# Kernel optimization log

Measured on AMD Instinct MI355X. Metric: run time of the kernel, lower is better.

Reference implementation:

```python
import jax, jax.numpy as jnp
import numpy as np

N_NODES = 100000
N_EDGES = 3200000
IN_CH = 128
HID = 128
ACT_DIM = 1


def _gcn_layer(x, W, b, src, dst, ew, n):
    # GCNConv with edge weights and self-loops already included in (src, dst, ew).
    # Symmetric normalization: norm_e = d^{-1/2}[src] * w_e * d^{-1/2}[dst]
    h = x @ W                                            # [N, F_out] dense transform first (cheap)
    deg = jax.ops.segment_sum(ew, dst, num_segments=n)   # weighted in-degree
    dinv = jnp.where(deg > 0, jax.lax.rsqrt(deg), 0.0)
    norm = dinv[src] * ew * dinv[dst]                    # [E]
    out = jax.ops.segment_sum(norm[:, None] * h[src], dst, num_segments=n)
    return out + b


def setup_inputs() -> dict:
    key = jax.random.key(0)
    ks = jax.random.split(key, 10)
    x = jax.random.normal(ks[0], (N_NODES, IN_CH), dtype=jnp.float32)
    edge_index = jax.random.randint(ks[1], (2, N_EDGES), 0, N_NODES, dtype=jnp.int64)
    edge_weight = jax.random.uniform(ks[2], (N_EDGES,), dtype=jnp.float32)
    action = jax.random.normal(ks[3], (N_NODES, ACT_DIM), dtype=jnp.float32)
    s1 = 1.0 / np.sqrt(IN_CH)
    s2 = 1.0 / np.sqrt(HID)
    s3 = 1.0 / np.sqrt(HID + ACT_DIM)
    W1 = jax.random.uniform(ks[4], (IN_CH, HID), jnp.float32, -s1, s1)
    b1 = jnp.zeros((HID,), jnp.float32)
    W2 = jax.random.uniform(ks[5], (HID, HID), jnp.float32, -s2, s2)
    b2 = jnp.zeros((HID,), jnp.float32)
    Wfc = jax.random.uniform(ks[6], (HID + ACT_DIM, 1), jnp.float32, -s3, s3)
    bfc = jax.random.uniform(ks[7], (1,), jnp.float32, -s3, s3)
    return {"x": x, "edge_index": edge_index, "edge_weight": edge_weight,
            "action": action, "W1": W1, "b1": b1, "W2": W2, "b2": b2,
            "Wfc": Wfc, "bfc": bfc}


def reference(x, edge_index, edge_weight, action, W1, b1, W2, b2, Wfc, bfc):
    n = x.shape[0]
    loop = jnp.arange(n, dtype=edge_index.dtype)
    src = jnp.concatenate([edge_index[0], loop])          # add self-loops
    dst = jnp.concatenate([edge_index[1], loop])
    ew = jnp.concatenate([edge_weight, jnp.ones((n,), edge_weight.dtype)])

    h = jax.nn.relu(_gcn_layer(x, W1, b1, src, dst, ew, n))
    h = jax.nn.relu(_gcn_layer(h, W2, b2, src, dst, ew, n))
    h = jnp.concatenate([h, action], axis=1)              # [N, HID+ACT_DIM]
    value = (h @ Wfc + bfc).squeeze()                     # [N]
    return value
```

## Files before the change

### kernel.cpp

```cpp
#include <hip/hip_runtime.h>
#include <hip/hip_bf16.h>
#include <stdint.h>

typedef unsigned short u16;
typedef uint32_t u32;
typedef unsigned long long u64;

__device__ __forceinline__ float bf2f(u16 u) {
    return __uint_as_float(((uint32_t)u) << 16);
}
__device__ __forceinline__ u16 f2bf(float f) {
    uint32_t u = __float_as_uint(f);
    uint32_t r = u + 0x7fffu + ((u >> 16) & 1u);
    return (u16)(r >> 16);
}

__device__ __forceinline__ float ldf(const float* p) { return *p; }
__device__ __forceinline__ float ldf(const u16* p) { return bf2f(*p); }

#define DEG_SCALE 4294967296.0f
#define DEG_INV 2.3283064365386963e-10f

#define BSHIFT 9
#define BSIZE 512
#define CAP 19456

__global__ void k_init0(u32* bwptr, int NB) {
    int t = threadIdx.x;
    if (t < NB) bwptr[t] = (u32)t * CAP;
}

template <typename TIn>
__device__ __forceinline__ void gemm_block(float* smem, const TIn* __restrict__ A,
                                           const float* __restrict__ W,
                                           u16* __restrict__ outp, int n, int bid) {
    float (*As)[128] = (float(*)[128])smem;
    float (*Ws)[128] = (float(*)[128])(smem + 32 * 128);
    int t = threadIdx.x;
    int row0 = bid * 32;

    if constexpr (sizeof(TIn) == 2) {
        for (int i = t; i < 32 * 64; i += 256) {
            int r = i >> 6, c2 = i & 63;
            int gr = row0 + r;
            uint32_t u = (gr < n) ? *reinterpret_cast<const uint32_t*>(&A[(size_t)gr * 128 + 2 * c2]) : 0u;
            As[r][2 * c2] = bf2f((u16)(u & 0xffff));
            As[r][2 * c2 + 1] = bf2f((u16)(u >> 16));
        }
    } else {
        for (int i = t; i < 32 * 128; i += 256) {
            int r = i >> 7, c = i & 127;
            int gr = row0 + r;
            As[r][c] = (gr < n) ? ldf(&A[(size_t)gr * 128 + c]) : 0.0f;
        }
    }

    float acc[4][4];
#pragma unroll
    for (int i = 0; i < 4; i++)
#pragma unroll
        for (int j = 0; j < 4; j++) acc[i][j] = 0.0f;

    int c0 = (t & 31) * 4;
    int r0 = (t >> 5) * 4;

    for (int kt = 0; kt < 128; kt += 32) {
        __syncthreads();
        for (int i = t; i < 32 * 128; i += 256) {
            int kk = i >> 7, c = i & 127;
            Ws[kk][c] = W[(size_t)(kt + kk) * 128 + c];
        }
        __syncthreads();
#pragma unroll
        for (int kk = 0; kk < 32; kk += 4) {
            float w0[4], w1[4], w2[4], w3[4];
            *(float4*)w0 = *(const float4*)&Ws[kk + 0][c0];
            *(float4*)w1 = *(const float4*)&Ws[kk + 1][c0];
            *(float4*)w2 = *(const float4*)&Ws[kk + 2][c0];
            *(float4*)w3 = *(const float4*)&Ws[kk + 3][c0];
#pragma unroll
            for (int i = 0; i < 4; i++) {
                float a[4];
                *(float4*)a = *(const float4*)&As[r0 + i][kt + kk];
#pragma unroll
                for (int j = 0; j < 4; j++) {
                    acc[i][j] = fmaf(a[0], w0[j], acc[i][j]);
                    acc[i][j] = fmaf(a[1], w1[j], acc[i][j]);
                    acc[i][j] = fmaf(a[2], w2[j], acc[i][j]);
                    acc[i][j] = fmaf(a[3], w3[j], acc[i][j]);
                }
            }
        }
    }

#pragma unroll
    for (int i = 0; i < 4; i++) {
        int gr = row0 + r0 + i;
        if (gr < n) {
            ushort4 o;
            o.x = f2bf(acc[i][0]);
            o.y = f2bf(acc[i][1]);
            o.z = f2bf(acc[i][2]);
            o.w = f2bf(acc[i][3]);
            *reinterpret_cast<ushort4*>(&outp[(size_t)gr * 128 + c0]) = o;
        }
    }
}

__global__ __launch_bounds__(256) void k_part_gemm(const float* __restrict__ x, const float* __restrict__ W1,
                                                   u16* __restrict__ tbuf, int n, int Gg,
                                                   const int* __restrict__ src, const int* __restrict__ dst,
                                                   const float* __restrict__ ew,
                                                   u32* bwptr, u64* __restrict__ ebuf,
                                                   int E, int EPB, int NB) {
    __shared__ float smem[2 * 32 * 128];
    int bid = blockIdx.x;
    int t = threadIdx.x;

    if (bid < Gg) gemm_block<float>(smem, x, W1, tbuf, n, bid);
    __syncthreads();

    u32* hist = (u32*)smem;
    u32* base = (u32*)smem + 256;
    if (t < NB) hist[t] = 0;
    __syncthreads();
    int e0 = bid * EPB;
    int e1 = min(e0 + EPB, E);
    if (e0 < E) {
        for (int e = e0 + t; e < e1; e += 256) {
            atomicAdd(&hist[dst[e] >> BSHIFT], 1u);
        }
        __syncthreads();
        if (t < NB) {
            base[t] = atomicAdd(&bwptr[t], hist[t]);
            hist[t] = 0;
        }
        __syncthreads();
        for (int e = e0 + t; e < e1; e += 256) {
            int d = dst[e];
            int b = d >> BSHIFT;
            u32 pos = base[b] + atomicAdd(&hist[b], 1u);
            u32 w0 = (u32)src[e] | ((u32)(d & (BSIZE - 1)) << 17);
            ebuf[pos] = (u64)w0 | ((u64)__float_as_uint(ew[e]) << 32);
        }
    }
}

__global__ __launch_bounds__(512) void k_bucket(const u64* __restrict__ ebuf, const u32* __restrict__ bwptr,
                                                u64* __restrict__ packed, float* __restrict__ dinv,
                                                int* __restrict__ rowptr, int n) {
    __shared__ u64 acc[BSIZE];
    __shared__ int sc[BSIZE];
    int b = blockIdx.x;
    int t = threadIdx.x;
    acc[t] = 0;
    __syncthreads();
    int cnt = (int)(bwptr[b] - (u32)b * CAP);
    const u64* eb = ebuf + (size_t)b * CAP;
    for (int e = t; e < cnt; e += 512) {
        u64 w = eb[e];
        int dlow = ((u32)w >> 17) & (BSIZE - 1);
        float wv = __uint_as_float((u32)(w >> 32));
        atomicAdd(&acc[dlow], (1ull << 48) | (u64)(wv * DEG_SCALE));
    }
    __syncthreads();
    u64 pk = acc[t] + (1ull << 32);
    int c = (int)(pk >> 48);
    sc[t] = c;
    __syncthreads();
    for (int off = 1; off < 512; off <<= 1) {
        int x = (t >= off) ? sc[t - off] : 0;
        __syncthreads();
        sc[t] += x;
        __syncthreads();
    }
    int node = (b << BSHIFT) + t;
    if (node < n) {
        packed[node] = pk;
        dinv[node] = rsqrtf((float)(pk & 0xFFFFFFFFFFFFull) * DEG_INV);
        rowptr[node] = b * CAP + (sc[t] - c);
    }
}

__global__ __launch_bounds__(512) void k_bscatter(const u64* __restrict__ ebuf, const u32* __restrict__ bwptr,
                                                  const int* __restrict__ rowptr, const float* __restrict__ dinv,
                                                  int2* __restrict__ rec, int n) {
    __shared__ u32 fill[BSIZE];
    __shared__ int rp[BSIZE];
    __shared__ float din[BSIZE];
    int b = blockIdx.x;
    int t = threadIdx.x;
    int node0 = b << BSHIFT;
    for (int i = t; i < BSIZE; i += 512) {
        int node = node0 + i;
        fill[i] = 0;
        rp[i] = (node < n) ? rowptr[node] : 0;
        din[i] = (node < n) ? dinv[node] : 0.f;
    }
    __syncthreads();
    int cnt = (int)(bwptr[b] - (u32)b * CAP);
    const u64* eb = ebuf + (size_t)b * CAP;
    for (int e = t; e < cnt; e += 512) {
        u64 w = eb[e];
        u32 lo = (u32)w;
        int s = lo & 0x1FFFF;
        int dlow = (lo >> 17) & (BSIZE - 1);
        float ewv = __uint_as_float((u32)(w >> 32));
        float nrm = dinv[s] * ewv * din[dlow];
        int pos = rp[dlow] + (int)atomicAdd(&fill[dlow], 1u);
        rec[pos] = make_int2(s, __float_as_int(nrm));
    }
}

template <typename TIn>
__global__ __launch_bounds__(256) void k_gemm(const TIn* __restrict__ A, const float* __restrict__ W,
                                              u16* __restrict__ outp, int n) {
    __shared__ float smem[2 * 32 * 128];
    gemm_block<TIn>(smem, A, W, outp, n, blockIdx.x);
}

template <int MODE>
__global__ __launch_bounds__(256) void k_agg(const u16* __restrict__ t, const int2* __restrict__ rec,
                                             const int* __restrict__ rowptr, const u64* __restrict__ packed,
                                             const float* __restrict__ dinv, const float* __restrict__ bias,
                                             u16* __restrict__ hout,
                                             const float* __restrict__ action, const float* __restrict__ Wfc,
                                             const float* __restrict__ bfc, float* __restrict__ out, int n) {
    int node = blockIdx.x * 4 + (threadIdx.x >> 6);
    if (node >= n) return;
    int lane = threadIdx.x & 63;
    int sl = lane >> 4;
    int c8 = (lane & 15) * 8;
    int base = rowptr[node];
    int m = (int)(packed[node] >> 48);

    float a0 = 0.f, a1 = 0.f, a2 = 0.f, a3 = 0.f, a4 = 0.f, a5 = 0.f, a6 = 0.f, a7 = 0.f;

#define ACCUM(G, NN)                                                         \
    {                                                                        \
        float nv = (NN);                                                     \
        a0 = fmaf(nv, __uint_as_float((G).x << 16), a0);                     \
        a1 = fmaf(nv, __uint_as_float((G).x & 0xFFFF0000u), a1);             \
        a2 = fmaf(nv, __uint_as_float((G).y << 16), a2);                     \
        a3 = fmaf(nv, __uint_as_float((G).y & 0xFFFF0000u), a3);             \
        a4 = fmaf(nv, __uint_as_float((G).z << 16), a4);                     \
        a5 = fmaf(nv, __uint_as_float((G).z & 0xFFFF0000u), a5);             \
        a6 = fmaf(nv, __uint_as_float((G).w << 16), a6);                     \
        a7 = fmaf(nv, __uint_as_float((G).w & 0xFFFF0000u), a7);             \
    }

    for (int e = 0; e < m; e += 8) {
        int e0 = e + sl;
        int e1 = e + 4 + sl;
        int2 r0 = (e0 < m) ? rec[base + e0] : make_int2(0, 0);
        int2 r1 = (e1 < m) ? rec[base + e1] : make_int2(0, 0);
        uint4 g0 = *reinterpret_cast<const uint4*>(t + (((u32)r0.x << 7) + c8));
        uint4 g1 = *reinterpret_cast<const uint4*>(t + (((u32)r1.x << 7) + c8));
        ACCUM(g0, __int_as_float(r0.y));
        ACCUM(g1, __int_as_float(r1.y));
    }
#undef ACCUM

#define RED(A)                                   \
    A += __shfl_xor(A, 16, 64);                  \
    A += __shfl_xor(A, 32, 64);
    RED(a0) RED(a1) RED(a2) RED(a3) RED(a4) RED(a5) RED(a6) RED(a7)
#undef RED

    if (sl == 0) {
        float di = dinv[node];
        float sdi = di * di;
        uint4 sv = *reinterpret_cast<const uint4*>(t + (((u32)node << 7) + c8));
        a0 = fmaf(sdi, __uint_as_float(sv.x << 16), a0);
        a1 = fmaf(sdi, __uint_as_float(sv.x & 0xFFFF0000u), a1);
        a2 = fmaf(sdi, __uint_as_float(sv.y << 16), a2);
        a3 = fmaf(sdi, __uint_as_float(sv.y & 0xFFFF0000u), a3);
        a4 = fmaf(sdi, __uint_as_float(sv.z << 16), a4);
        a5 = fmaf(sdi, __uint_as_float(sv.z & 0xFFFF0000u), a5);
        a6 = fmaf(sdi, __uint_as_float(sv.w << 16), a6);
        a7 = fmaf(sdi, __uint_as_float(sv.w & 0xFFFF0000u), a7);
        float4 b0 = *reinterpret_cast<const float4*>(&bias[c8]);
        float4 b1 = *reinterpret_cast<const float4*>(&bias[c8 + 4]);
        a0 = fmaxf(a0 + b0.x, 0.f); a1 = fmaxf(a1 + b0.y, 0.f);
        a2 = fmaxf(a2 + b0.z, 0.f); a3 = fmaxf(a3 + b0.w, 0.f);
        a4 = fmaxf(a4 + b1.x, 0.f); a5 = fmaxf(a5 + b1.y, 0.f);
        a6 = fmaxf(a6 + b1.z, 0.f); a7 = fmaxf(a7 + b1.w, 0.f);
        if (MODE == 0) {
            uint4 o;
            o.x = (u32)f2bf(a0) | ((u32)f2bf(a1) << 16);
            o.y = (u32)f2bf(a2) | ((u32)f2bf(a3) << 16);
            o.z = (u32)f2bf(a4) | ((u32)f2bf(a5) << 16);
            o.w = (u32)f2bf(a6) | ((u32)f2bf(a7) << 16);
            *reinterpret_cast<uint4*>(hout + (((u32)node << 7) + c8)) = o;
        } else {
            float4 w0 = *reinterpret_cast<const float4*>(&Wfc[c8]);
            float4 w1 = *reinterpret_cast<const float4*>(&Wfc[c8 + 4]);
            float v = a0 * w0.x + a1 * w0.y + a2 * w0.z + a3 * w0.w +
                      a4 * w1.x + a5 * w1.y + a6 * w1.z + a7 * w1.w;
            v += __shfl_xor(v, 1, 64);
            v += __shfl_xor(v, 2, 64);
            v += __shfl_xor(v, 4, 64);
            v += __shfl_xor(v, 8, 64);
            if (lane == 0) out[node] = v + action[node] * Wfc[128] + bfc[0];
        }
    }
}

extern "C" void kernel_launch(void* const* d_in, const int* in_sizes, int n_in,
                              void* d_out, int out_size, void* d_ws, size_t ws_size,
                              hipStream_t stream) {
    const float* x = (const float*)d_in[0];
    const int* ei = (const int*)d_in[1];
    const float* ew = (const float*)d_in[2];
    const float* action = (const float*)d_in[3];
    const float* W1 = (const float*)d_in[4];
    const float* b1 = (const float*)d_in[5];
    const float* W2 = (const float*)d_in[6];
    const float* b2 = (const float*)d_in[7];
    const float* Wfc = (const float*)d_in[8];
    const float* bfc = (const float*)d_in[9];
    float* out = (float*)d_out;

    int n = in_sizes[0] / 128;
    int E = in_sizes[2];
    const int* src = ei;
    const int* dst = ei + E;

    char* p = (char*)d_ws;
    auto carve = [&](size_t bytes) -> char* {
        char* q = p;
        p += (bytes + 255) & ~(size_t)255;
        return q;
    };
    int NB = (n + BSIZE - 1) >> BSHIFT;
    u64* packed = (u64*)carve((size_t)n * 8);
    float* dinv = (float*)carve((size_t)n * 4);
    int* rowptr = (int*)carve((size_t)n * 4);
    u32* bwptr = (u32*)carve((size_t)NB * 4);
    u64* ebuf = (u64*)carve((size_t)NB * CAP * 8);
    int2* rec = (int2*)carve((size_t)NB * CAP * 8);
    u16* tbuf = (u16*)carve((size_t)n * 128 * 2);
    u16* hbuf = (u16*)carve((size_t)n * 128 * 2);

    int Gg = (n + 31) / 32;
    int EPB = (E + Gg - 1) / Gg;

    k_init0<<<1, 256, 0, stream>>>(bwptr, NB);
    k_part_gemm<<<Gg, 256, 0, stream>>>(x, W1, tbuf, n, Gg, src, dst, ew,
                                        bwptr, ebuf, E, EPB, NB);
    k_bucket<<<NB, 512, 0, stream>>>(ebuf, bwptr, packed, dinv, rowptr, n);
    k_bscatter<<<NB, 512, 0, stream>>>(ebuf, bwptr, rowptr, dinv, rec, n);

    k_agg<0><<<(n + 3) / 4, 256, 0, stream>>>(tbuf, rec, rowptr, packed, dinv, b1, hbuf,
                                              nullptr, nullptr, nullptr, nullptr, n);
    k_gemm<u16><<<Gg, 256, 0, stream>>>(hbuf, W2, tbuf, n);
    k_agg<1><<<(n + 3) / 4, 256, 0, stream>>>(tbuf, rec, rowptr, packed, dinv, b2, nullptr,
                                              action, Wfc, bfc, out, n);
}
```

Baseline: 567.9 us.

## Slice GEMM output into 16-column panels and split aggregation across feature slices

The transformed feature buffer is now stored as eight column-major panels of 16 bf16 features per node, so each aggregation block handles one 16-feature slice and the gathered working set per pass is 3.2 MB instead of 25.6 MB. The aim is to keep the random gathers in cache. The final layer reduces partial dot products with atomicAdd into an output zeroed by a new kernel. The partition kernel now interleaves GEMM and edge-bucketing blocks rather than running both in every block. In exchange, rec/rowptr are read eight times, the grid is eight times larger, and the final sum order depends on atomic ordering.

```diff
diff --git a/kernel.cpp b/kernel.cpp
--- a/kernel.cpp
+++ b/kernel.cpp
@@ -25,15 +25,16 @@
 #define BSIZE 512
 #define CAP 19456
 
-__global__ void k_init0(u32* bwptr, int NB) {
-    int t = threadIdx.x;
-    if (t < NB) bwptr[t] = (u32)t * CAP;
+__global__ void k_zero(float* out, int n, u32* bwptr, int NB) {
+    int i = blockIdx.x * 256 + threadIdx.x;
+    if (i < n) out[i] = 0.0f;
+    if (blockIdx.x == 0 && threadIdx.x < NB) bwptr[threadIdx.x] = (u32)threadIdx.x * CAP;
 }
 
 template <typename TIn>
 __device__ __forceinline__ void gemm_block(float* smem, const TIn* __restrict__ A,
                                            const float* __restrict__ W,
-                                           u16* __restrict__ outp, int n, int bid) {
+                                           u16* __restrict__ outp, int n, int n16, int bid) {
     float (*As)[128] = (float(*)[128])smem;
     float (*Ws)[128] = (float(*)[128])(smem + 32 * 128);
     int t = threadIdx.x;
@@ -93,6 +94,7 @@
         }
     }
 
+    u16* obase = outp + (size_t)(c0 >> 4) * n16 + (c0 & 15);
 #pragma unroll
     for (int i = 0; i < 4; i++) {
         int gr = row0 + r0 + i;
@@ -102,13 +104,13 @@
             o.y = f2bf(acc[i][1]);
             o.z = f2bf(acc[i][2]);
             o.w = f2bf(acc[i][3]);
-            *reinterpret_cast<ushort4*>(&outp[(size_t)gr * 128 + c0]) = o;
+            *reinterpret_cast<ushort4*>(obase + (size_t)gr * 16) = o;
         }
     }
 }
 
 __global__ __launch_bounds__(256) void k_part_gemm(const float* __restrict__ x, const float* __restrict__ W1,
-                                                   u16* __restrict__ tbuf, int n, int Gg,
+                                                   u16* __restrict__ tbuf, int n, int n16, int Gg,
                                                    const int* __restrict__ src, const int* __restrict__ dst,
                                                    const float* __restrict__ ew,
                                                    u32* bwptr, u64* __restrict__ ebuf,
@@ -116,33 +118,34 @@
     __shared__ float smem[2 * 32 * 128];
     int bid = blockIdx.x;
     int t = threadIdx.x;
-
-    if (bid < Gg) gemm_block<float>(smem, x, W1, tbuf, n, bid);
-    __syncthreads();
-
+    if ((bid & 1) == 0) {
+        int gb = bid >> 1;
+        if (gb < Gg) gemm_block<float>(smem, x, W1, tbuf, n, n16, gb);
+        return;
+    }
+    int pb = bid >> 1;
     u32* hist = (u32*)smem;
     u32* base = (u32*)smem + 256;
     if (t < NB) hist[t] = 0;
     __syncthreads();
-    int e0 = bid * EPB;
+    int e0 = pb * EPB;
     int e1 = min(e0 + EPB, E);
-    if (e0 < E) {
-        for (int e = e0 + t; e < e1; e += 256) {
-            atomicAdd(&hist[dst[e] >> BSHIFT], 1u);
-        }
-        __syncthreads();
-        if (t < NB) {
-            base[t] = atomicAdd(&bwptr[t], hist[t]);
-            hist[t] = 0;
-        }
-        __syncthreads();
-        for (int e = e0 + t; e < e1; e += 256) {
-            int d = dst[e];
-            int b = d >> BSHIFT;
-            u32 pos = base[b] + atomicAdd(&hist[b], 1u);
-            u32 w0 = (u32)src[e] | ((u32)(d & (BSIZE - 1)) << 17);
-            ebuf[pos] = (u64)w0 | ((u64)__float_as_uint(ew[e]) << 32);
-        }
+    if (e0 >= E) return;
+    for (int e = e0 + t; e < e1; e += 256) {
+        atomicAdd(&hist[dst[e] >> BSHIFT], 1u);
+    }
+    __syncthreads();
+    if (t < NB) {
+        base[t] = atomicAdd(&bwptr[t], hist[t]);
+        hist[t] = 0;
+    }
+    __syncthreads();
+    for (int e = e0 + t; e < e1; e += 256) {
+        int d = dst[e];
+        int b = d >> BSHIFT;
+        u32 pos = base[b] + atomicAdd(&hist[b], 1u);
+        u32 w0 = (u32)src[e] | ((u32)(d & (BSIZE - 1)) << 17);
+        ebuf[pos] = (u64)w0 | ((u64)__float_as_uint(ew[e]) << 32);
     }
 }
 
@@ -214,9 +217,9 @@
 
 template <typename TIn>
 __global__ __launch_bounds__(256) void k_gemm(const TIn* __restrict__ A, const float* __restrict__ W,
-                                              u16* __restrict__ outp, int n) {
+                                              u16* __restrict__ outp, int n, int n16) {
     __shared__ float smem[2 * 32 * 128];
-    gemm_block<TIn>(smem, A, W, outp, n, blockIdx.x);
+    gemm_block<TIn>(smem, A, W, outp, n, n16, blockIdx.x);
 }
 
 template <int MODE>
@@ -225,12 +228,17 @@
                                              const float* __restrict__ dinv, const float* __restrict__ bias,
                                              u16* __restrict__ hout,
                                              const float* __restrict__ action, const float* __restrict__ Wfc,
-                                             const float* __restrict__ bfc, float* __restrict__ out, int n) {
-    int node = blockIdx.x * 4 + (threadIdx.x >> 6);
+                                             const float* __restrict__ bfc, float* __restrict__ out,
+                                             int n, int n16) {
+    int bid = blockIdx.x;
+    int s = bid & 7;
+    int g = bid >> 3;
+    int node = g * 4 + (threadIdx.x >> 6);
     if (node >= n) return;
     int lane = threadIdx.x & 63;
-    int sl = lane >> 4;
-    int c8 = (lane & 15) * 8;
+    int slot = lane >> 1;
+    int h = lane & 1;
+    const u16* ts = t + (size_t)s * n16;
     int base = rowptr[node];
     int m = (int)(packed[node] >> 48);
 
@@ -249,38 +257,30 @@
         a7 = fmaf(nv, __uint_as_float((G).w & 0xFFFF0000u), a7);             \
     }
 
-    for (int e = 0; e < m; e += 8) {
-        int e0 = e + sl;
-        int e1 = e + 4 + sl;
-        int2 r0 = (e0 < m) ? rec[base + e0] : make_int2(0, 0);
-        int2 r1 = (e1 < m) ? rec[base + e1] : make_int2(0, 0);
-        uint4 g0 = *reinterpret_cast<const uint4*>(t + (((u32)r0.x << 7) + c8));
-        uint4 g1 = *reinterpret_cast<const uint4*>(t + (((u32)r1.x << 7) + c8));
-        ACCUM(g0, __int_as_float(r0.y));
-        ACCUM(g1, __int_as_float(r1.y));
-    }
-#undef ACCUM
+    for (int e = 0; e < m; e += 32) {
+        int ei = e + slot;
+        int2 r = (ei < m) ? rec[base + ei] : make_int2(0, 0);
+        uint4 gv = *reinterpret_cast<const uint4*>(ts + ((u32)r.x * 16 + h * 8));
+        ACCUM(gv, __int_as_float(r.y));
+    }
 
 #define RED(A)                                   \
+    A += __shfl_xor(A, 2, 64);                   \
+    A += __shfl_xor(A, 4, 64);                   \
+    A += __shfl_xor(A, 8, 64);                   \
     A += __shfl_xor(A, 16, 64);                  \
     A += __shfl_xor(A, 32, 64);
     RED(a0) RED(a1) RED(a2) RED(a3) RED(a4) RED(a5) RED(a6) RED(a7)
 #undef RED
 
-    if (sl == 0) {
+    if (slot == 0) {
         float di = dinv[node];
         float sdi = di * di;
-        uint4 sv = *reinterpret_cast<const uint4*>(t + (((u32)node << 7) + c8));
-        a0 = fmaf(sdi, __uint_as_float(sv.x << 16), a0);
-        a1 = fmaf(sdi, __uint_as_float(sv.x & 0xFFFF0000u), a1);
-        a2 = fmaf(sdi, __uint_as_float(sv.y << 16), a2);
-        a3 = fmaf(sdi, __uint_as_float(sv.y & 0xFFFF0000u), a3);
-        a4 = fmaf(sdi, __uint_as_float(sv.z << 16), a4);
-        a5 = fmaf(sdi, __uint_as_float(sv.z & 0xFFFF0000u), a5);
-        a6 = fmaf(sdi, __uint_as_float(sv.w << 16), a6);
-        a7 = fmaf(sdi, __uint_as_float(sv.w & 0xFFFF0000u), a7);
-        float4 b0 = *reinterpret_cast<const float4*>(&bias[c8]);
-        float4 b1 = *reinterpret_cast<const float4*>(&bias[c8 + 4]);
+        uint4 sv = *reinterpret_cast<const uint4*>(ts + ((u32)node * 16 + h * 8));
+        ACCUM(sv, sdi);
+        int cb = s * 16 + h * 8;
+        float4 b0 = *reinterpret_cast<const float4*>(&bias[cb]);
+        float4 b1 = *reinterpret_cast<const float4*>(&bias[cb + 4]);
         a0 = fmaxf(a0 + b0.x, 0.f); a1 = fmaxf(a1 + b0.y, 0.f);
         a2 = fmaxf(a2 + b0.z, 0.f); a3 = fmaxf(a3 + b0.w, 0.f);
         a4 = fmaxf(a4 + b1.x, 0.f); a5 = fmaxf(a5 + b1.y, 0.f);
@@ -291,19 +291,20 @@
             o.y = (u32)f2bf(a2) | ((u32)f2bf(a3) << 16);
             o.z = (u32)f2bf(a4) | ((u32)f2bf(a5) << 16);
             o.w = (u32)f2bf(a6) | ((u32)f2bf(a7) << 16);
-            *reinterpret_cast<uint4*>(hout + (((u32)node << 7) + c8)) = o;
+            *reinterpret_cast<uint4*>(hout + (size_t)node * 128 + cb) = o;
         } else {
-            float4 w0 = *reinterpret_cast<const float4*>(&Wfc[c8]);
-            float4 w1 = *reinterpret_cast<const float4*>(&Wfc[c8 + 4]);
+            float4 w0 = *reinterpret_cast<const float4*>(&Wfc[cb]);
+            float4 w1 = *reinterpret_cast<const float4*>(&Wfc[cb + 4]);
             float v = a0 * w0.x + a1 * w0.y + a2 * w0.z + a3 * w0.w +
                       a4 * w1.x + a5 * w1.y + a6 * w1.z + a7 * w1.w;
             v += __shfl_xor(v, 1, 64);
-            v += __shfl_xor(v, 2, 64);
-            v += __shfl_xor(v, 4, 64);
-            v += __shfl_xor(v, 8, 64);
-            if (lane == 0) out[node] = v + action[node] * Wfc[128] + bfc[0];
-        }
-    }
+            if (lane == 0) {
+                float extra = (s == 0) ? action[node] * Wfc[128] + bfc[0] : 0.f;
+                atomicAdd(&out[node], v + extra);
+            }
+        }
+    }
+#undef ACCUM
 }
 
 extern "C" void kernel_launch(void* const* d_in, const int* in_sizes, int n_in,
@@ -325,6 +326,7 @@
     int E = in_sizes[2];
     const int* src = ei;
     const int* dst = ei + E;
+    int n16 = n * 16;
 
     char* p = (char*)d_ws;
     auto carve = [&](size_t bytes) -> char* {
@@ -345,15 +347,16 @@
     int Gg = (n + 31) / 32;
     int EPB = (E + Gg - 1) / Gg;
 
-    k_init0<<<1, 256, 0, stream>>>(bwptr, NB);
-    k_part_gemm<<<Gg, 256, 0, stream>>>(x, W1, tbuf, n, Gg, src, dst, ew,
-                                        bwptr, ebuf, E, EPB, NB);
+    k_zero<<<(n + 255) / 256, 256, 0, stream>>>(out, n, bwptr, NB);
+    k_part_gemm<<<2 * Gg, 256, 0, stream>>>(x, W1, tbuf, n, n16, Gg, src, dst, ew,
+                                            bwptr, ebuf, E, EPB, NB);
     k_bucket<<<NB, 512, 0, stream>>>(ebuf, bwptr, packed, dinv, rowptr, n);
     k_bscatter<<<NB, 512, 0, stream>>>(ebuf, bwptr, rowptr, dinv, rec, n);
 
-    k_agg<0><<<(n + 3) / 4, 256, 0, stream>>>(tbuf, rec, rowptr, packed, dinv, b1, hbuf,
-                                              nullptr, nullptr, nullptr, nullptr, n);
-    k_gemm<u16><<<Gg, 256, 0, stream>>>(hbuf, W2, tbuf, n);
-    k_agg<1><<<(n + 3) / 4, 256, 0, stream>>>(tbuf, rec, rowptr, packed, dinv, b2, nullptr,
-                                              action, Wfc, bfc, out, n);
-}
+    int aggGrid = 8 * ((n + 3) / 4);
+    k_agg<0><<<aggGrid, 256, 0, stream>>>(tbuf, rec, rowptr, packed, dinv, b1, hbuf,
+                                          nullptr, nullptr, nullptr, nullptr, n, n16);
+    k_gemm<u16><<<Gg, 256, 0, stream>>>(hbuf, W2, tbuf, n, n16);
+    k_agg<1><<<aggGrid, 256, 0, stream>>>(tbuf, rec, rowptr, packed, dinv, b2, nullptr,
+                                          action, Wfc, bfc, out, n, n16);
+}
```

Result: slower. 1.068 ms (+88.1%).

## Split GEMM and partition blocks, use 16-lane groups per node in aggregation

Applied to the files above, without the earlier changes.

The fused first kernel no longer makes every block run a GEMM tile and then an edge-partition pass. Blocks are now interleaved 3:2 into pure GEMM blocks and pure partition blocks, so the two kinds of work run concurrently on different CUs instead of serially within one block. The aggregation kernels now give each node a 16-lane group that walks all of its edges with 4-way unrolled gathers, replacing 64 lanes split into 4 edge slices. This removes the cross-slice shuffle reduction and the idle lanes in the epilogue. The trade-off is less memory-level parallelism per node and load imbalance for high-degree nodes, since 16 lanes now walk the whole edge list.

```diff
diff --git a/kernel.cpp b/kernel.cpp
--- a/kernel.cpp
+++ b/kernel.cpp
@@ -115,34 +115,37 @@
                                                    int E, int EPB, int NB) {
     __shared__ float smem[2 * 32 * 128];
     int bid = blockIdx.x;
-    int t = threadIdx.x;
-
-    if (bid < Gg) gemm_block<float>(smem, x, W1, tbuf, n, bid);
-    __syncthreads();
-
+    int g = bid / 5;
+    int r = bid - g * 5;
+    if (r < 3) {
+        int gb = 3 * g + r;
+        if (gb < Gg) gemm_block<float>(smem, x, W1, tbuf, n, gb);
+        return;
+    }
+    int pb = 2 * g + (r - 3);
     u32* hist = (u32*)smem;
     u32* base = (u32*)smem + 256;
+    int t = threadIdx.x;
     if (t < NB) hist[t] = 0;
     __syncthreads();
-    int e0 = bid * EPB;
+    int e0 = pb * EPB;
     int e1 = min(e0 + EPB, E);
-    if (e0 < E) {
-        for (int e = e0 + t; e < e1; e += 256) {
-            atomicAdd(&hist[dst[e] >> BSHIFT], 1u);
-        }
-        __syncthreads();
-        if (t < NB) {
-            base[t] = atomicAdd(&bwptr[t], hist[t]);
-            hist[t] = 0;
-        }
-        __syncthreads();
-        for (int e = e0 + t; e < e1; e += 256) {
-            int d = dst[e];
-            int b = d >> BSHIFT;
-            u32 pos = base[b] + atomicAdd(&hist[b], 1u);
-            u32 w0 = (u32)src[e] | ((u32)(d & (BSIZE - 1)) << 17);
-            ebuf[pos] = (u64)w0 | ((u64)__float_as_uint(ew[e]) << 32);
-        }
+    if (e0 >= E) return;
+    for (int e = e0 + t; e < e1; e += 256) {
+        atomicAdd(&hist[dst[e] >> BSHIFT], 1u);
+    }
+    __syncthreads();
+    if (t < NB) {
+        base[t] = atomicAdd(&bwptr[t], hist[t]);
+        hist[t] = 0;
+    }
+    __syncthreads();
+    for (int e = e0 + t; e < e1; e += 256) {
+        int d = dst[e];
+        int b = d >> BSHIFT;
+        u32 pos = base[b] + atomicAdd(&hist[b], 1u);
+        u32 w0 = (u32)src[e] | ((u32)(d & (BSIZE - 1)) << 17);
+        ebuf[pos] = (u64)w0 | ((u64)__float_as_uint(ew[e]) << 32);
     }
 }
 
@@ -226,11 +229,10 @@
                                              u16* __restrict__ hout,
                                              const float* __restrict__ action, const float* __restrict__ Wfc,
                                              const float* __restrict__ bfc, float* __restrict__ out, int n) {
-    int node = blockIdx.x * 4 + (threadIdx.x >> 6);
+    int node = blockIdx.x * 16 + (threadIdx.x >> 4);
     if (node >= n) return;
-    int lane = threadIdx.x & 63;
-    int sl = lane >> 4;
-    int c8 = (lane & 15) * 8;
+    int gl = threadIdx.x & 15;
+    int c8 = gl * 8;
     int base = rowptr[node];
     int m = (int)(packed[node] >> 48);
 
@@ -249,60 +251,57 @@
         a7 = fmaf(nv, __uint_as_float((G).w & 0xFFFF0000u), a7);             \
     }
 
-    for (int e = 0; e < m; e += 8) {
-        int e0 = e + sl;
-        int e1 = e + 4 + sl;
-        int2 r0 = (e0 < m) ? rec[base + e0] : make_int2(0, 0);
-        int2 r1 = (e1 < m) ? rec[base + e1] : make_int2(0, 0);
+    int e = 0;
+    for (; e + 4 <= m; e += 4) {
+        int2 r0 = rec[base + e + 0];
+        int2 r1 = rec[base + e + 1];
+        int2 r2 = rec[base + e + 2];
+        int2 r3 = rec[base + e + 3];
         uint4 g0 = *reinterpret_cast<const uint4*>(t + (((u32)r0.x << 7) + c8));
         uint4 g1 = *reinterpret_cast<const uint4*>(t + (((u32)r1.x << 7) + c8));
+        uint4 g2 = *reinterpret_cast<const uint4*>(t + (((u32)r2.x << 7) + c8));
+        uint4 g3 = *reinterpret_cast<const uint4*>(t + (((u32)r3.x << 7) + c8));
         ACCUM(g0, __int_as_float(r0.y));
         ACCUM(g1, __int_as_float(r1.y));
-    }
+        ACCUM(g2, __int_as_float(r2.y));
+        ACCUM(g3, __int_as_float(r3.y));
+    }
+    for (; e < m; e++) {
+        int2 r = rec[base + e];
+        uint4 g = *reinterpret_cast<const uint4*>(t + (((u32)r.x << 7) + c8));
+        ACCUM(g, __int_as_float(r.y));
+    }
+
+    float di = dinv[node];
+    float sdi = di * di;
+    uint4 sv = *reinterpret_cast<const uint4*>(t + (((u32)node << 7) + c8));
+    ACCUM(sv, sdi);
 #undef ACCUM
 
-#define RED(A)                                   \
-    A += __shfl_xor(A, 16, 64);                  \
-    A += __shfl_xor(A, 32, 64);
-    RED(a0) RED(a1) RED(a2) RED(a3) RED(a4) RED(a5) RED(a6) RED(a7)
-#undef RED
-
-    if (sl == 0) {
-        float di = dinv[node];
-        float sdi = di * di;
-        uint4 sv = *reinterpret_cast<const uint4*>(t + (((u32)node << 7) + c8));
-        a0 = fmaf(sdi, __uint_as_float(sv.x << 16), a0);
-        a1 = fmaf(sdi, __uint_as_float(sv.x & 0xFFFF0000u), a1);
-        a2 = fmaf(sdi, __uint_as_float(sv.y << 16), a2);
-        a3 = fmaf(sdi, __uint_as_float(sv.y & 0xFFFF0000u), a3);
-        a4 = fmaf(sdi, __uint_as_float(sv.z << 16), a4);
-        a5 = fmaf(sdi, __uint_as_float(sv.z & 0xFFFF0000u), a5);
-        a6 = fmaf(sdi, __uint_as_float(sv.w << 16), a6);
-        a7 = fmaf(sdi, __uint_as_float(sv.w & 0xFFFF0000u), a7);
-        float4 b0 = *reinterpret_cast<const float4*>(&bias[c8]);
-        float4 b1 = *reinterpret_cast<const float4*>(&bias[c8 + 4]);
-        a0 = fmaxf(a0 + b0.x, 0.f); a1 = fmaxf(a1 + b0.y, 0.f);
-        a2 = fmaxf(a2 + b0.z, 0.f); a3 = fmaxf(a3 + b0.w, 0.f);
-        a4 = fmaxf(a4 + b1.x, 0.f); a5 = fmaxf(a5 + b1.y, 0.f);
-        a6 = fmaxf(a6 + b1.z, 0.f); a7 = fmaxf(a7 + b1.w, 0.f);
-        if (MODE == 0) {
-            uint4 o;
-            o.x = (u32)f2bf(a0) | ((u32)f2bf(a1) << 16);
-            o.y = (u32)f2bf(a2) | ((u32)f2bf(a3) << 16);
-            o.z = (u32)f2bf(a4) | ((u32)f2bf(a5) << 16);
-            o.w = (u32)f2bf(a6) | ((u32)f2bf(a7) << 16);
-            *reinterpret_cast<uint4*>(hout + (((u32)node << 7) + c8)) = o;
-        } else {
-            float4 w0 = *reinterpret_cast<const float4*>(&Wfc[c8]);
-            float4 w1 = *reinterpret_cast<const float4*>(&Wfc[c8 + 4]);
-            float v = a0 * w0.x + a1 * w0.y + a2 * w0.z + a3 * w0.w +
-                      a4 * w1.x + a5 * w1.y + a6 * w1.z + a7 * w1.w;
-            v += __shfl_xor(v, 1, 64);
-            v += __shfl_xor(v, 2, 64);
-            v += __shfl_xor(v, 4, 64);
-            v += __shfl_xor(v, 8, 64);
-            if (lane == 0) out[node] = v + action[node] * Wfc[128] + bfc[0];
-        }
+    float4 b0 = *reinterpret_cast<const float4*>(&bias[c8]);
+    float4 b1 = *reinterpret_cast<const float4*>(&bias[c8 + 4]);
+    a0 = fmaxf(a0 + b0.x, 0.f); a1 = fmaxf(a1 + b0.y, 0.f);
+    a2 = fmaxf(a2 + b0.z, 0.f); a3 = fmaxf(a3 + b0.w, 0.f);
+    a4 = fmaxf(a4 + b1.x, 0.f); a5 = fmaxf(a5 + b1.y, 0.f);
+    a6 = fmaxf(a6 + b1.z, 0.f); a7 = fmaxf(a7 + b1.w, 0.f);
+
+    if (MODE == 0) {
+        uint4 o;
+        o.x = (u32)f2bf(a0) | ((u32)f2bf(a1) << 16);
+        o.y = (u32)f2bf(a2) | ((u32)f2bf(a3) << 16);
+        o.z = (u32)f2bf(a4) | ((u32)f2bf(a5) << 16);
+        o.w = (u32)f2bf(a6) | ((u32)f2bf(a7) << 16);
+        *reinterpret_cast<uint4*>(hout + (((u32)node << 7) + c8)) = o;
+    } else {
+        float4 w0 = *reinterpret_cast<const float4*>(&Wfc[c8]);
+        float4 w1 = *reinterpret_cast<const float4*>(&Wfc[c8 + 4]);
+        float v = a0 * w0.x + a1 * w0.y + a2 * w0.z + a3 * w0.w +
+                  a4 * w1.x + a5 * w1.y + a6 * w1.z + a7 * w1.w;
+        v += __shfl_xor(v, 1, 64);
+        v += __shfl_xor(v, 2, 64);
+        v += __shfl_xor(v, 4, 64);
+        v += __shfl_xor(v, 8, 64);
+        if (gl == 0) out[node] = v + action[node] * Wfc[128] + bfc[0];
     }
 }
 
@@ -343,17 +342,19 @@
     u16* hbuf = (u16*)carve((size_t)n * 128 * 2);
 
     int Gg = (n + 31) / 32;
-    int EPB = (E + Gg - 1) / Gg;
+    int G = (Gg + 2) / 3;
+    int Gp = 2 * G;
+    int EPB = (E + Gp - 1) / Gp;
 
     k_init0<<<1, 256, 0, stream>>>(bwptr, NB);
-    k_part_gemm<<<Gg, 256, 0, stream>>>(x, W1, tbuf, n, Gg, src, dst, ew,
-                                        bwptr, ebuf, E, EPB, NB);
+    k_part_gemm<<<G * 5, 256, 0, stream>>>(x, W1, tbuf, n, Gg, src, dst, ew,
+                                           bwptr, ebuf, E, EPB, NB);
     k_bucket<<<NB, 512, 0, stream>>>(ebuf, bwptr, packed, dinv, rowptr, n);
     k_bscatter<<<NB, 512, 0, stream>>>(ebuf, bwptr, rowptr, dinv, rec, n);
 
-    k_agg<0><<<(n + 3) / 4, 256, 0, stream>>>(tbuf, rec, rowptr, packed, dinv, b1, hbuf,
-                                              nullptr, nullptr, nullptr, nullptr, n);
+    k_agg<0><<<(n + 15) / 16, 256, 0, stream>>>(tbuf, rec, rowptr, packed, dinv, b1, hbuf,
+                                                nullptr, nullptr, nullptr, nullptr, n);
     k_gemm<u16><<<Gg, 256, 0, stream>>>(hbuf, W2, tbuf, n);
-    k_agg<1><<<(n + 3) / 4, 256, 0, stream>>>(tbuf, rec, rowptr, packed, dinv, b2, nullptr,
-                                              action, Wfc, bfc, out, n);
-}
+    k_agg<1><<<(n + 15) / 16, 256, 0, stream>>>(tbuf, rec, rowptr, packed, dinv, b2, nullptr,
+                                                action, Wfc, bfc, out, n);
+}
```

Result: faster. 547.4 us (-3.6%).
